# Performance work log

Hardware: AMD Instinct MI355X
Metric: run time of the kernel (lower is better)

## Reference

```python
import jax, jax.numpy as jnp
import numpy as np

D = 1024
H = 16
HD = D // H
B = 4
N = 2048


def setup_inputs() -> dict:
    key = jax.random.key(0)
    ks = jax.random.split(key, 5)
    x = jax.random.normal(ks[0], (B, N, D), dtype=jnp.float32)
    # nn.Linear(D, 3D): weight [3D, D], bias [3D]; y = x @ W.T + b
    w_qkv = jax.random.normal(ks[1], (3 * D, D), dtype=jnp.float32) * (1.0 / np.sqrt(D))
    b_qkv = jax.random.normal(ks[2], (3 * D,), dtype=jnp.float32) * 0.02
    w_out = jax.random.normal(ks[3], (D, D), dtype=jnp.float32) * (1.0 / np.sqrt(D))
    b_out = jax.random.normal(ks[4], (D,), dtype=jnp.float32) * 0.02
    return {"x": x, "w_qkv": w_qkv, "b_qkv": b_qkv, "w_out": w_out, "b_out": b_out}


def reference(x, w_qkv, b_qkv, w_out, b_out):
    Bn, Nn, Dn = x.shape
    scale = HD ** (-0.5)
    qkv = x @ w_qkv.T + b_qkv                      # [B, N, 3D]
    q, k, v = jnp.split(qkv, 3, axis=-1)
    # [B, N, D] -> [B, H, N, HD]
    def heads(t):
        return t.reshape(Bn, Nn, H, HD).transpose(0, 2, 1, 3)
    q, k, v = heads(q), heads(k), heads(v)
    scores = jnp.einsum('bhqd,bhkd->bhqk', q, k) * scale   # [B, H, N, N]
    causal = jnp.tril(jnp.ones((Nn, Nn), dtype=bool))
    scores = jnp.where(causal[None, None], scores, jnp.float32(-jnp.inf))
    alpha = jax.nn.softmax(scores, axis=-1)
    out = jnp.einsum('bhqk,bhkd->bhqd', alpha, v)          # [B, H, N, HD]
    out = out.transpose(0, 2, 1, 3).reshape(Bn, Nn, Dn)
    return out @ w_out.T + b_out
```

## Files before the change

kernel.cpp:

```cpp
#include <hip/hip_runtime.h>
#include <hip/hip_bf16.h>

#define D_MODEL 1024
#define H_HEADS 16
#define HD 64
#define B_BATCH 4
#define N_SEQ 2048
#define BH (B_BATCH*H_HEADS)
#define M_TOT (B_BATCH*N_SEQ)
#define N_QKV (3*D_MODEL)
#define QSCALE 0.18033688011112042f

typedef __bf16 bf16x8 __attribute__((ext_vector_type(8)));
typedef __bf16 bf16x4 __attribute__((ext_vector_type(4)));
typedef float f32x4 __attribute__((ext_vector_type(4)));

#define MFMA16 __builtin_amdgcn_mfma_f32_16x16x32_bf16

__device__ inline ushort cvt_bf16(float f){
  return __builtin_bit_cast(ushort, (__bf16)f);
}

#define GLOAD_LDS16(g, l) __builtin_amdgcn_global_load_lds( \
    (const __attribute__((address_space(1))) void*)(g), \
    (__attribute__((address_space(3))) void*)(l), 16, 0, 0)

__global__ void cvt_f32_bf16_kernel(const float* __restrict__ src, ushort* __restrict__ dst, int n){
  int i = (blockIdx.x*blockDim.x + threadIdx.x)*4;
  int stride = gridDim.x*blockDim.x*4;
  for (; i < n; i += stride){
    float4 f = *reinterpret_cast<const float4*>(src+i);
    ushort4 u;
    u.x=cvt_bf16(f.x); u.y=cvt_bf16(f.y); u.z=cvt_bf16(f.z); u.w=cvt_bf16(f.w);
    *reinterpret_cast<ushort4*>(dst+i) = u;
  }
}

template<int MODE, int MR>
__global__ __launch_bounds__(512,1) void gemm4p(
    const ushort* __restrict__ A, const ushort* __restrict__ Wt,
    const float* __restrict__ bias, void* __restrict__ out,
    int M, int Ncols, int K)
{
  constexpr int BM = MR*32;
  constexpr int BN = 256;
  constexpr int A_SR = BM/2;
  constexpr int A_ISS = BM/128;
  constexpr int VN = 2*A_ISS + 2;
  __shared__ __align__(16) ushort As[2][2][A_SR][64];
  __shared__ __align__(16) ushort Bs[2][2][128][64];
  const int tid = threadIdx.x;
  const int w = tid>>6, lane = tid&63;
  const int wm = w>>2, wn = w&3;
  const int lr = lane&15, lk = lane>>4;

  const int nx = Ncols/BN;
  const int q8 = gridDim.x>>3;
  const int gid = (blockIdx.x&7)*q8 + (blockIdx.x>>3);
  const int bx = gid % nx, by = gid / nx;
  const int row0 = by*BM, col0 = bx*BN;

  const int s_sr8 = lane>>3;
  const int s_cl  = (lane&7) ^ s_sr8;
  const int s_dr  = s_cl>>2;
  const int s_dc  = (s_cl&3)*8;

  auto stageA = [&](int buf, int kt, int ks){
    #pragma unroll
    for (int i=0;i<A_ISS;i++){
      const int sr0 = (w*A_ISS + i)*8;
      GLOAD_LDS16(&A[(size_t)(row0 + 2*(sr0 + s_sr8) + s_dr)*K + kt*64 + ks*32 + s_dc],
                  &As[buf][ks][sr0][0]);
    }
  };
  auto stageB = [&](int buf, int kt, int ks){
    #pragma unroll
    for (int i=0;i<2;i++){
      const int sr0 = (w*2 + i)*8;
      GLOAD_LDS16(&Wt[(size_t)(col0 + 2*(sr0 + s_sr8) + s_dr)*K + kt*64 + ks*32 + s_dc],
                  &Bs[buf][ks][sr0][0]);
    }
  };

  const int rdc = (((lr&1)*4 + lk) ^ ((lr>>1)&7)) * 8;
  f32x4 acc[MR][4] = {};

  const int NT = K/64;
  stageA(0,0,0); stageB(0,0,0); stageA(0,0,1); stageB(0,0,1);
  stageA(1,1,0); stageB(1,1,0); stageA(1,1,1);
  asm volatile("s_waitcnt vmcnt(%0)" :: "i"(VN) : "memory");
  __builtin_amdgcn_s_barrier();

  for (int kt=0; kt<NT; ++kt){
    const int cur = kt&1, nb = cur^1;
    bf16x8 af[MR], bfr[2];

    #pragma unroll
    for (int m=0;m<MR;m++)
      af[m] = *reinterpret_cast<const bf16x8*>(&As[cur][0][wm*(MR*8) + m*8 + (lr>>1)][rdc]);
    bfr[0] = *reinterpret_cast<const bf16x8*>(&Bs[cur][0][wn*32 + 0*8 + (lr>>1)][rdc]);
    bfr[1] = *reinterpret_cast<const bf16x8*>(&Bs[cur][0][wn*32 + 1*8 + (lr>>1)][rdc]);
    if (kt+1 < NT) stageB(nb, kt+1, 1);
    __builtin_amdgcn_s_barrier();
    asm volatile("s_waitcnt lgkmcnt(0)" ::: "memory");
    __builtin_amdgcn_sched_barrier(0);
    __builtin_amdgcn_s_setprio(1);
    #pragma unroll
    for (int m=0;m<MR;m++){
      acc[m][0] = MFMA16(af[m], bfr[0], acc[m][0], 0,0,0);
      acc[m][1] = MFMA16(af[m], bfr[1], acc[m][1], 0,0,0);
    }
    __builtin_amdgcn_s_setprio(0);
    __builtin_amdgcn_s_barrier();

    bfr[0] = *reinterpret_cast<const bf16x8*>(&Bs[cur][0][wn*32 + 2*8 + (lr>>1)][rdc]);
    bfr[1] = *reinterpret_cast<const bf16x8*>(&Bs[cur][0][wn*32 + 3*8 + (lr>>1)][rdc]);
    if (kt+2 < NT) stageA(cur, kt+2, 0);
    __builtin_amdgcn_s_barrier();
    asm volatile("s_waitcnt lgkmcnt(0)" ::: "memory");
    __builtin_amdgcn_sched_barrier(0);
    __builtin_amdgcn_s_setprio(1);
    #pragma unroll
    for (int m=0;m<MR;m++){
      acc[m][2] = MFMA16(af[m], bfr[0], acc[m][2], 0,0,0);
      acc[m][3] = MFMA16(af[m], bfr[1], acc[m][3], 0,0,0);
    }
    __builtin_amdgcn_s_setprio(0);
    __builtin_amdgcn_s_barrier();

    #pragma unroll
    for (int m=0;m<MR;m++)
      af[m] = *reinterpret_cast<const bf16x8*>(&As[cur][1][wm*(MR*8) + m*8 + (lr>>1)][rdc]);
    bfr[0] = *reinterpret_cast<const bf16x8*>(&Bs[cur][1][wn*32 + 0*8 + (lr>>1)][rdc]);
    bfr[1] = *reinterpret_cast<const bf16x8*>(&Bs[cur][1][wn*32 + 1*8 + (lr>>1)][rdc]);
    if (kt+2 < NT) stageB(cur, kt+2, 0);
    __builtin_amdgcn_s_barrier();
    asm volatile("s_waitcnt lgkmcnt(0)" ::: "memory");
    __builtin_amdgcn_sched_barrier(0);
    __builtin_amdgcn_s_setprio(1);
    #pragma unroll
    for (int m=0;m<MR;m++){
      acc[m][0] = MFMA16(af[m], bfr[0], acc[m][0], 0,0,0);
      acc[m][1] = MFMA16(af[m], bfr[1], acc[m][1], 0,0,0);
    }
    __builtin_amdgcn_s_setprio(0);
    __builtin_amdgcn_s_barrier();

    bfr[0] = *reinterpret_cast<const bf16x8*>(&Bs[cur][1][wn*32 + 2*8 + (lr>>1)][rdc]);
    bfr[1] = *reinterpret_cast<const bf16x8*>(&Bs[cur][1][wn*32 + 3*8 + (lr>>1)][rdc]);
    if (kt+2 < NT) stageA(cur, kt+2, 1);
    __builtin_amdgcn_s_barrier();
    asm volatile("s_waitcnt lgkmcnt(0)" ::: "memory");
    __builtin_amdgcn_sched_barrier(0);
    __builtin_amdgcn_s_setprio(1);
    #pragma unroll
    for (int m=0;m<MR;m++){
      acc[m][2] = MFMA16(af[m], bfr[0], acc[m][2], 0,0,0);
      acc[m][3] = MFMA16(af[m], bfr[1], acc[m][3], 0,0,0);
    }
    __builtin_amdgcn_s_setprio(0);
    if (kt < NT-2) asm volatile("s_waitcnt vmcnt(%0)" :: "i"(VN) : "memory");
    else           asm volatile("s_waitcnt vmcnt(0)" ::: "memory");
    __builtin_amdgcn_s_barrier();
  }

  const int ocol_base = col0 + wn*64;
  #pragma unroll
  for (int m=0;m<MR;m++){
    #pragma unroll
    for(int n=0;n<4;n++){
      const int gc = ocol_base + n*16 + lr;
      const float bv = bias[gc];
      const int gr0 = row0 + wm*(MR*16) + m*16 + lk*4;
      float vals[4];
      #pragma unroll
      for (int r=0;r<4;r++) vals[r] = acc[m][n][r] + bv;
      if (MODE==0){
        const int which = gc >> 10;
        const int d = gc & 1023;
        const int h = d >> 6, hd = d & 63;
        const int b = gr0 >> 11, nn0 = gr0 & 2047;
        ushort* o = (ushort*)out;
        if (which==2){
          ushort4 u;
          u.x=cvt_bf16(vals[0]); u.y=cvt_bf16(vals[1]);
          u.z=cvt_bf16(vals[2]); u.w=cvt_bf16(vals[3]);
          *reinterpret_cast<ushort4*>(
            &o[2ull*BH*N_SEQ*HD + ((size_t)(b*H_HEADS+h)*HD + hd)*N_SEQ + nn0]) = u;
        } else {
          const float sc = (which==0) ? QSCALE : 1.0f;
          #pragma unroll
          for (int r=0;r<4;r++)
            o[(size_t)which*((size_t)BH*N_SEQ*HD)
              + ((size_t)(b*H_HEADS+h)*N_SEQ + nn0 + r)*HD + hd] = cvt_bf16(vals[r]*sc);
        }
      } else {
        #pragma unroll
        for (int r=0;r<4;r++)
          ((float*)out)[(size_t)(gr0+r)*Ncols + gc] = vals[r];
      }
    }
  }
}

__global__ __launch_bounds__(256,3) void attn_mfma(
    const ushort* __restrict__ q, const ushort* __restrict__ kg, const ushort* __restrict__ vtg,
    ushort* __restrict__ attn_out)
{
  __shared__ __align__(16) ushort Ks[2][64][64];
  __shared__ __align__(16) ushort Vs[2][64][64];
  __shared__ __align__(16) ushort Ps[4][32][72];
  const int tid=threadIdx.x, w=tid>>6, lane=tid&63;
  const int lr=lane&15, lk=lane>>4;
  const int bid = blockIdx.x;
  const int strip = 15 - (bid>>6);
  const int bh = bid & 63;
  const size_t base=(size_t)bh*N_SEQ*HD;
  const ushort* kb = kg + base;
  const ushort* vb = vtg + base;
  const int b = bh>>4, h = bh&15;

  const int s_roff = lane>>3;
  const int s_g    = (lane&7) ^ s_roff;
  int rd_base[2];
  #pragma unroll
  for (int ks=0;ks<2;ks++)
    rd_base[ks] = lr*64 + (((ks*4+lk) ^ (lr&7))*8);

  const int row0 = strip*128;
  const int wrow = row0 + w*32;
  const int nt = 2*strip + 2;

  bf16x8 qf[2][2];
  #pragma unroll
  for (int qt=0;qt<2;qt++)
    #pragma unroll
    for (int ks=0;ks<2;ks++)
      qf[qt][ks] = *reinterpret_cast<const bf16x8*>(
          &q[base + (size_t)(wrow + qt*16 + lr)*HD + ks*32 + lk*8]);

  f32x4 o_acc[2][4] = {};
  float mrun[2] = {-1e30f,-1e30f}, lrun[2] = {0.f,0.f};

  {
    const int r0k = w*16, rA = r0k + s_roff;
    GLOAD_LDS16(&kb[(size_t)(rA)*HD + s_g*8],       &Ks[0][r0k][0]);
    GLOAD_LDS16(&kb[(size_t)(rA+8)*HD + s_g*8],     &Ks[0][r0k+8][0]);
    GLOAD_LDS16(&vb[(size_t)(rA)*N_SEQ + s_g*8],    &Vs[0][r0k][0]);
    GLOAD_LDS16(&vb[(size_t)(rA+8)*N_SEQ + s_g*8],  &Vs[0][r0k+8][0]);
  }
  int cur = 0;
  for (int t=0;t<nt;t++){
    __syncthreads();
    if (t+1 < nt){
      const int j1 = (t+1)*64;
      const int r0k = w*16, rA = r0k + s_roff;
      GLOAD_LDS16(&kb[(size_t)(j1+rA)*HD + s_g*8],        &Ks[cur^1][r0k][0]);
      GLOAD_LDS16(&kb[(size_t)(j1+rA+8)*HD + s_g*8],      &Ks[cur^1][r0k+8][0]);
      GLOAD_LDS16(&vb[(size_t)(rA)*N_SEQ + j1 + s_g*8],   &Vs[cur^1][r0k][0]);
      GLOAD_LDS16(&vb[(size_t)(rA+8)*N_SEQ + j1 + s_g*8], &Vs[cur^1][r0k+8][0]);
    }
    const int j0 = t*64;
    if (j0 <= wrow + 31){
      const ushort* Kt = &Ks[cur][0][0];
      const ushort* Vt = &Vs[cur][0][0];
      f32x4 sacc[2][4] = {};
      __builtin_amdgcn_s_setprio(1);
      #pragma unroll
      for (int ks=0;ks<2;ks++)
        #pragma unroll
        for (int kt=0;kt<4;kt++){
          bf16x8 kf = *reinterpret_cast<const bf16x8*>(Kt + kt*1024 + rd_base[ks]);
          sacc[0][kt] = MFMA16(kf, qf[0][ks], sacc[0][kt], 0,0,0);
          sacc[1][kt] = MFMA16(kf, qf[1][ks], sacc[1][kt], 0,0,0);
        }
      __builtin_amdgcn_s_setprio(0);

      const bool tailmask = (j0 + 63 > wrow);
      #pragma unroll
      for (int qt=0;qt<2;qt++){
        const int qrow = wrow + qt*16 + lr;
        if (tailmask){
          #pragma unroll
          for (int kt=0;kt<4;kt++)
            #pragma unroll
            for (int r=0;r<4;r++)
              if (j0 + kt*16 + lk*4 + r > qrow) sacc[qt][kt][r] = -1e30f;
        }
        float mx = -1e30f;
        #pragma unroll
        for (int kt=0;kt<4;kt++)
          #pragma unroll
          for (int r=0;r<4;r++) mx = fmaxf(mx, sacc[qt][kt][r]);
        mx = fmaxf(mx, __shfl_xor(mx, 16));
        mx = fmaxf(mx, __shfl_xor(mx, 32));
        float mcur = mrun[qt];
        if (__any(mx - mcur > 8.0f)){
          const float mnew = fmaxf(mcur, mx);
          const float corr = exp2f(mcur - mnew);
          mrun[qt] = mnew; mcur = mnew;
          lrun[qt] *= corr;
          #pragma unroll
          for (int dt=0;dt<4;dt++) o_acc[qt][dt] *= corr;
        }
        float sum = 0.f;
        #pragma unroll
        for (int kt=0;kt<4;kt++){
          float p0 = exp2f(sacc[qt][kt][0]-mcur);
          float p1 = exp2f(sacc[qt][kt][1]-mcur);
          float p2 = exp2f(sacc[qt][kt][2]-mcur);
          float p3 = exp2f(sacc[qt][kt][3]-mcur);
          sum += (p0+p1)+(p2+p3);
          bf16x4 pk;
          pk[0]=(__bf16)p0; pk[1]=(__bf16)p1; pk[2]=(__bf16)p2; pk[3]=(__bf16)p3;
          *reinterpret_cast<bf16x4*>(&Ps[w][qt*16+lr][kt*16+lk*4]) = pk;
        }
        lrun[qt] += sum;
      }

      #pragma unroll
      for (int ks=0;ks<2;ks++){
        bf16x8 pa0 = *reinterpret_cast<const bf16x8*>(&Ps[w][lr][ks*32+lk*8]);
        bf16x8 pa1 = *reinterpret_cast<const bf16x8*>(&Ps[w][16+lr][ks*32+lk*8]);
        __builtin_amdgcn_s_setprio(1);
        #pragma unroll
        for (int dt=0;dt<4;dt++){
          bf16x8 vf = *reinterpret_cast<const bf16x8*>(Vt + dt*1024 + rd_base[ks]);
          o_acc[0][dt] = MFMA16(vf, pa0, o_acc[0][dt], 0,0,0);
          o_acc[1][dt] = MFMA16(vf, pa1, o_acc[1][dt], 0,0,0);
        }
        __builtin_amdgcn_s_setprio(0);
      }
    }
    cur ^= 1;
  }

  #pragma unroll
  for (int qt=0;qt<2;qt++){
    float rl = lrun[qt];
    rl += __shfl_xor(rl, 16);
    rl += __shfl_xor(rl, 32);
    const float rinv = 1.0f / rl;
    const size_t rowb = ((size_t)(b*N_SEQ) + wrow + qt*16 + lr)*D_MODEL + h*HD;
    #pragma unroll
    for (int dt=0;dt<4;dt++){
      bf16x4 u;
      u[0]=(__bf16)(o_acc[qt][dt][0]*rinv);
      u[1]=(__bf16)(o_acc[qt][dt][1]*rinv);
      u[2]=(__bf16)(o_acc[qt][dt][2]*rinv);
      u[3]=(__bf16)(o_acc[qt][dt][3]*rinv);
      *reinterpret_cast<bf16x4*>(&attn_out[rowb + dt*16 + lk*4]) = u;
    }
  }
}

extern "C" void kernel_launch(void* const* d_in, const int* in_sizes, int n_in,
                              void* d_out, int out_size, void* d_ws, size_t ws_size,
                              hipStream_t stream){
  const float* x     = (const float*)d_in[0];
  const float* w_qkv = (const float*)d_in[1];
  const float* b_qkv = (const float*)d_in[2];
  const float* w_out = (const float*)d_in[3];
  const float* b_out = (const float*)d_in[4];

  char* ws = (char*)d_ws;
  size_t off = 0;
  ushort* x_bf    = (ushort*)(ws+off); off += (size_t)M_TOT*D_MODEL*2;
  ushort* wqkv_bf = (ushort*)(ws+off); off += (size_t)N_QKV*D_MODEL*2;
  ushort* wout_bf = (ushort*)(ws+off); off += (size_t)D_MODEL*D_MODEL*2;
  ushort* qkv     = (ushort*)(ws+off); off += 3ull*BH*N_SEQ*HD*2;
  ushort* attn_o  = (ushort*)(ws+off); off += (size_t)M_TOT*D_MODEL*2;

  cvt_f32_bf16_kernel<<<1024, 256, 0, stream>>>(x,     x_bf,    M_TOT*D_MODEL);
  cvt_f32_bf16_kernel<<<512,  256, 0, stream>>>(w_qkv, wqkv_bf, N_QKV*D_MODEL);
  cvt_f32_bf16_kernel<<<256,  256, 0, stream>>>(w_out, wout_bf, D_MODEL*D_MODEL);

  gemm4p<0,8><<<384, 512, 0, stream>>>(x_bf, wqkv_bf, b_qkv, qkv, M_TOT, N_QKV, D_MODEL);

  const ushort* qb  = qkv;
  const ushort* kb  = qkv + (size_t)BH*N_SEQ*HD;
  const ushort* vtb = qkv + 2ull*BH*N_SEQ*HD;
  attn_mfma<<<1024, 256, 0, stream>>>(qb, kb, vtb, attn_o);

  gemm4p<2,4><<<256, 512, 0, stream>>>(attn_o, wout_bf, b_out, (float*)d_out, M_TOT, D_MODEL, D_MODEL);
}
```

Before: 189.0 us.

## Switch GEMMs to 32x32x16 MFMA with a simpler double-buffered pipeline

Rewrites both projection GEMMs to use 32x32x16 bf16 MFMA tiles instead of 16x16x32. Each 32x32 output tile needs fewer LDS fragment loads per unit of compute. The K-loop drops from four barrier-separated quarter phases with two-tile prefetch to a two-buffer scheme that prefetches the next K tile while computing the current one, with a single full vmcnt(0) wait per tile. Launch bounds now request two blocks per CU. The risk is less memory latency hiding from the shallower prefetch depth and higher register pressure from the larger accumulators.

```diff
diff --git a/kernel.cpp b/kernel.cpp
--- a/kernel.cpp
+++ b/kernel.cpp
@@ -14,8 +14,10 @@
 typedef __bf16 bf16x8 __attribute__((ext_vector_type(8)));
 typedef __bf16 bf16x4 __attribute__((ext_vector_type(4)));
 typedef float f32x4 __attribute__((ext_vector_type(4)));
+typedef float f32x16 __attribute__((ext_vector_type(16)));
 
 #define MFMA16 __builtin_amdgcn_mfma_f32_16x16x32_bf16
+#define MFMA32 __builtin_amdgcn_mfma_f32_32x32x16_bf16
 
 __device__ inline ushort cvt_bf16(float f){
   return __builtin_bit_cast(ushort, (__bf16)f);
@@ -36,23 +38,21 @@
   }
 }
 
-template<int MODE, int MR>
-__global__ __launch_bounds__(512,1) void gemm4p(
+template<int MODE, int MRT>
+__global__ __launch_bounds__(512,2) void gemm2p(
     const ushort* __restrict__ A, const ushort* __restrict__ Wt,
     const float* __restrict__ bias, void* __restrict__ out,
     int M, int Ncols, int K)
 {
-  constexpr int BM = MR*32;
+  constexpr int BM = MRT*64;
   constexpr int BN = 256;
   constexpr int A_SR = BM/2;
   constexpr int A_ISS = BM/128;
-  constexpr int VN = 2*A_ISS + 2;
   __shared__ __align__(16) ushort As[2][2][A_SR][64];
   __shared__ __align__(16) ushort Bs[2][2][128][64];
   const int tid = threadIdx.x;
   const int w = tid>>6, lane = tid&63;
   const int wm = w>>2, wn = w&3;
-  const int lr = lane&15, lk = lane>>4;
 
   const int nx = Ncols/BN;
   const int q8 = gridDim.x>>3;
@@ -82,122 +82,131 @@
     }
   };
 
-  const int rdc = (((lr&1)*4 + lk) ^ ((lr>>1)&7)) * 8;
-  f32x4 acc[MR][4] = {};
-
+  const int rsr = (lane&31)>>1;
+  const int swz = rsr & 7;
+  const int pk0 = ((((lane&1)<<2) + 0 + (lane>>5)) ^ swz) * 8;
+  const int pk1 = ((((lane&1)<<2) + 2 + (lane>>5)) ^ swz) * 8;
+
+  f32x16 acc[MRT][2] = {};
   const int NT = K/64;
+
   stageA(0,0,0); stageB(0,0,0); stageA(0,0,1); stageB(0,0,1);
-  stageA(1,1,0); stageB(1,1,0); stageA(1,1,1);
-  asm volatile("s_waitcnt vmcnt(%0)" :: "i"(VN) : "memory");
+  asm volatile("s_waitcnt vmcnt(0)" ::: "memory");
   __builtin_amdgcn_s_barrier();
 
-  for (int kt=0; kt<NT; ++kt){
-    const int cur = kt&1, nb = cur^1;
-    bf16x8 af[MR], bfr[2];
-
-    #pragma unroll
-    for (int m=0;m<MR;m++)
-      af[m] = *reinterpret_cast<const bf16x8*>(&As[cur][0][wm*(MR*8) + m*8 + (lr>>1)][rdc]);
-    bfr[0] = *reinterpret_cast<const bf16x8*>(&Bs[cur][0][wn*32 + 0*8 + (lr>>1)][rdc]);
-    bfr[1] = *reinterpret_cast<const bf16x8*>(&Bs[cur][0][wn*32 + 1*8 + (lr>>1)][rdc]);
-    if (kt+1 < NT) stageB(nb, kt+1, 1);
-    __builtin_amdgcn_s_barrier();
+  auto ktbody = [&](int cur, int kt) __attribute__((always_inline)) {
+    const int nb = cur^1;
+    const ushort* Ab0 = &As[cur][0][0][0];
+    const ushort* Ab1 = &As[cur][1][0][0];
+    const ushort* Bb0 = &Bs[cur][0][0][0];
+    const ushort* Bb1 = &Bs[cur][1][0][0];
+    bf16x8 A0[MRT], A1[MRT], B0[2], B1[2];
+    bf16x8 C0[MRT], C1[MRT], D0[2], D1[2];
+    #pragma unroll
+    for (int mt=0;mt<MRT;mt++){
+      const int ao = (wm*(MRT*16) + mt*16 + rsr)*64;
+      A0[mt] = *reinterpret_cast<const bf16x8*>(Ab0 + ao + pk0);
+      A1[mt] = *reinterpret_cast<const bf16x8*>(Ab0 + ao + pk1);
+    }
+    #pragma unroll
+    for (int nt=0;nt<2;nt++){
+      const int bo = (wn*32 + nt*16 + rsr)*64;
+      B0[nt] = *reinterpret_cast<const bf16x8*>(Bb0 + bo + pk0);
+      B1[nt] = *reinterpret_cast<const bf16x8*>(Bb0 + bo + pk1);
+    }
+    if (kt+1 < NT){ stageA(nb, kt+1, 0); stageB(nb, kt+1, 0); }
+    asm volatile("s_waitcnt lgkmcnt(0)" ::: "memory");
+    __builtin_amdgcn_sched_barrier(0);
+    #pragma unroll
+    for (int mt=0;mt<MRT;mt++){
+      const int ao = (wm*(MRT*16) + mt*16 + rsr)*64;
+      C0[mt] = *reinterpret_cast<const bf16x8*>(Ab1 + ao + pk0);
+      C1[mt] = *reinterpret_cast<const bf16x8*>(Ab1 + ao + pk1);
+    }
+    #pragma unroll
+    for (int nt=0;nt<2;nt++){
+      const int bo = (wn*32 + nt*16 + rsr)*64;
+      D0[nt] = *reinterpret_cast<const bf16x8*>(Bb1 + bo + pk0);
+      D1[nt] = *reinterpret_cast<const bf16x8*>(Bb1 + bo + pk1);
+    }
+    if (kt+1 < NT){ stageA(nb, kt+1, 1); stageB(nb, kt+1, 1); }
+    __builtin_amdgcn_sched_barrier(0);
+    __builtin_amdgcn_s_setprio(1);
+    #pragma unroll
+    for (int mt=0;mt<MRT;mt++){
+      acc[mt][0] = MFMA32(A0[mt], B0[0], acc[mt][0], 0,0,0);
+      acc[mt][1] = MFMA32(A0[mt], B0[1], acc[mt][1], 0,0,0);
+    }
+    #pragma unroll
+    for (int mt=0;mt<MRT;mt++){
+      acc[mt][0] = MFMA32(A1[mt], B1[0], acc[mt][0], 0,0,0);
+      acc[mt][1] = MFMA32(A1[mt], B1[1], acc[mt][1], 0,0,0);
+    }
+    __builtin_amdgcn_s_setprio(0);
     asm volatile("s_waitcnt lgkmcnt(0)" ::: "memory");
     __builtin_amdgcn_sched_barrier(0);
     __builtin_amdgcn_s_setprio(1);
     #pragma unroll
-    for (int m=0;m<MR;m++){
-      acc[m][0] = MFMA16(af[m], bfr[0], acc[m][0], 0,0,0);
-      acc[m][1] = MFMA16(af[m], bfr[1], acc[m][1], 0,0,0);
+    for (int mt=0;mt<MRT;mt++){
+      acc[mt][0] = MFMA32(C0[mt], D0[0], acc[mt][0], 0,0,0);
+      acc[mt][1] = MFMA32(C0[mt], D0[1], acc[mt][1], 0,0,0);
+    }
+    #pragma unroll
+    for (int mt=0;mt<MRT;mt++){
+      acc[mt][0] = MFMA32(C1[mt], D1[0], acc[mt][0], 0,0,0);
+      acc[mt][1] = MFMA32(C1[mt], D1[1], acc[mt][1], 0,0,0);
     }
     __builtin_amdgcn_s_setprio(0);
+    asm volatile("s_waitcnt vmcnt(0)" ::: "memory");
     __builtin_amdgcn_s_barrier();
-
-    bfr[0] = *reinterpret_cast<const bf16x8*>(&Bs[cur][0][wn*32 + 2*8 + (lr>>1)][rdc]);
-    bfr[1] = *reinterpret_cast<const bf16x8*>(&Bs[cur][0][wn*32 + 3*8 + (lr>>1)][rdc]);
-    if (kt+2 < NT) stageA(cur, kt+2, 0);
-    __builtin_amdgcn_s_barrier();
-    asm volatile("s_waitcnt lgkmcnt(0)" ::: "memory");
-    __builtin_amdgcn_sched_barrier(0);
-    __builtin_amdgcn_s_setprio(1);
-    #pragma unroll
-    for (int m=0;m<MR;m++){
-      acc[m][2] = MFMA16(af[m], bfr[0], acc[m][2], 0,0,0);
-      acc[m][3] = MFMA16(af[m], bfr[1], acc[m][3], 0,0,0);
-    }
-    __builtin_amdgcn_s_setprio(0);
-    __builtin_amdgcn_s_barrier();
-
-    #pragma unroll
-    for (int m=0;m<MR;m++)
-      af[m] = *reinterpret_cast<const bf16x8*>(&As[cur][1][wm*(MR*8) + m*8 + (lr>>1)][rdc]);
-    bfr[0] = *reinterpret_cast<const bf16x8*>(&Bs[cur][1][wn*32 + 0*8 + (lr>>1)][rdc]);
-    bfr[1] = *reinterpret_cast<const bf16x8*>(&Bs[cur][1][wn*32 + 1*8 + (lr>>1)][rdc]);
-    if (kt+2 < NT) stageB(cur, kt+2, 0);
-    __builtin_amdgcn_s_barrier();
-    asm volatile("s_waitcnt lgkmcnt(0)" ::: "memory");
-    __builtin_amdgcn_sched_barrier(0);
-    __builtin_amdgcn_s_setprio(1);
-    #pragma unroll
-    for (int m=0;m<MR;m++){
-      acc[m][0] = MFMA16(af[m], bfr[0], acc[m][0], 0,0,0);
-      acc[m][1] = MFMA16(af[m], bfr[1], acc[m][1], 0,0,0);
-    }
-    __builtin_amdgcn_s_setprio(0);
-    __builtin_amdgcn_s_barrier();
-
-    bfr[0] = *reinterpret_cast<const bf16x8*>(&Bs[cur][1][wn*32 + 2*8 + (lr>>1)][rdc]);
-    bfr[1] = *reinterpret_cast<const bf16x8*>(&Bs[cur][1][wn*32 + 3*8 + (lr>>1)][rdc]);
-    if (kt+2 < NT) stageA(cur, kt+2, 1);
-    __builtin_amdgcn_s_barrier();
-    asm volatile("s_waitcnt lgkmcnt(0)" ::: "memory");
-    __builtin_amdgcn_sched_barrier(0);
-    __builtin_amdgcn_s_setprio(1);
-    #pragma unroll
-    for (int m=0;m<MR;m++){
-      acc[m][2] = MFMA16(af[m], bfr[0], acc[m][2], 0,0,0);
-      acc[m][3] = MFMA16(af[m], bfr[1], acc[m][3], 0,0,0);
-    }
-    __builtin_amdgcn_s_setprio(0);
-    if (kt < NT-2) asm volatile("s_waitcnt vmcnt(%0)" :: "i"(VN) : "memory");
-    else           asm volatile("s_waitcnt vmcnt(0)" ::: "memory");
-    __builtin_amdgcn_s_barrier();
-  }
-
-  const int ocol_base = col0 + wn*64;
+  };
+
+  for (int kt=0; kt<NT; kt+=2){
+    ktbody(0, kt);
+    ktbody(1, kt+1);
+  }
+
   #pragma unroll
-  for (int m=0;m<MR;m++){
-    #pragma unroll
-    for(int n=0;n<4;n++){
-      const int gc = ocol_base + n*16 + lr;
+  for (int mt=0;mt<MRT;mt++){
+    #pragma unroll
+    for (int nt=0;nt<2;nt++){
+      const int gc = col0 + wn*64 + nt*32 + (lane&31);
       const float bv = bias[gc];
-      const int gr0 = row0 + wm*(MR*16) + m*16 + lk*4;
-      float vals[4];
-      #pragma unroll
-      for (int r=0;r<4;r++) vals[r] = acc[m][n][r] + bv;
+      const int grB = row0 + wm*(MRT*32) + mt*32 + 4*(lane>>5);
       if (MODE==0){
         const int which = gc >> 10;
         const int d = gc & 1023;
         const int h = d >> 6, hd = d & 63;
-        const int b = gr0 >> 11, nn0 = gr0 & 2047;
         ushort* o = (ushort*)out;
-        if (which==2){
-          ushort4 u;
-          u.x=cvt_bf16(vals[0]); u.y=cvt_bf16(vals[1]);
-          u.z=cvt_bf16(vals[2]); u.w=cvt_bf16(vals[3]);
-          *reinterpret_cast<ushort4*>(
-            &o[2ull*BH*N_SEQ*HD + ((size_t)(b*H_HEADS+h)*HD + hd)*N_SEQ + nn0]) = u;
-        } else {
-          const float sc = (which==0) ? QSCALE : 1.0f;
+        #pragma unroll
+        for (int rg=0;rg<4;rg++){
+          const int gr0 = grB + rg*8;
+          const int b = gr0 >> 11, nn0 = gr0 & 2047;
+          if (which==2){
+            ushort4 u;
+            u.x=cvt_bf16(acc[mt][nt][rg*4+0] + bv);
+            u.y=cvt_bf16(acc[mt][nt][rg*4+1] + bv);
+            u.z=cvt_bf16(acc[mt][nt][rg*4+2] + bv);
+            u.w=cvt_bf16(acc[mt][nt][rg*4+3] + bv);
+            *reinterpret_cast<ushort4*>(
+              &o[2ull*BH*N_SEQ*HD + ((size_t)(b*H_HEADS+h)*HD + hd)*N_SEQ + nn0]) = u;
+          } else {
+            const float sc = (which==0) ? QSCALE : 1.0f;
+            #pragma unroll
+            for (int r=0;r<4;r++)
+              o[(size_t)which*((size_t)BH*N_SEQ*HD)
+                + ((size_t)(b*H_HEADS+h)*N_SEQ + nn0 + r)*HD + hd]
+                  = cvt_bf16((acc[mt][nt][rg*4+r] + bv)*sc);
+          }
+        }
+      } else {
+        #pragma unroll
+        for (int rg=0;rg<4;rg++){
+          const int gr0 = grB + rg*8;
           #pragma unroll
           for (int r=0;r<4;r++)
-            o[(size_t)which*((size_t)BH*N_SEQ*HD)
-              + ((size_t)(b*H_HEADS+h)*N_SEQ + nn0 + r)*HD + hd] = cvt_bf16(vals[r]*sc);
-        }
-      } else {
-        #pragma unroll
-        for (int r=0;r<4;r++)
-          ((float*)out)[(size_t)(gr0+r)*Ncols + gc] = vals[r];
+            ((float*)out)[(size_t)(gr0+r)*Ncols + gc] = acc[mt][nt][rg*4+r] + bv;
+        }
       }
     }
   }
@@ -375,12 +384,12 @@
   cvt_f32_bf16_kernel<<<512,  256, 0, stream>>>(w_qkv, wqkv_bf, N_QKV*D_MODEL);
   cvt_f32_bf16_kernel<<<256,  256, 0, stream>>>(w_out, wout_bf, D_MODEL*D_MODEL);
 
-  gemm4p<0,8><<<384, 512, 0, stream>>>(x_bf, wqkv_bf, b_qkv, qkv, M_TOT, N_QKV, D_MODEL);
+  gemm2p<0,4><<<384, 512, 0, stream>>>(x_bf, wqkv_bf, b_qkv, qkv, M_TOT, N_QKV, D_MODEL);
 
   const ushort* qb  = qkv;
   const ushort* kb  = qkv + (size_t)BH*N_SEQ*HD;
   const ushort* vtb = qkv + 2ull*BH*N_SEQ*HD;
   attn_mfma<<<1024, 256, 0, stream>>>(qb, kb, vtb, attn_o);
 
-  gemm4p<2,4><<<256, 512, 0, stream>>>(attn_o, wout_bf, b_out, (float*)d_out, M_TOT, D_MODEL, D_MODEL);
-}
+  gemm2p<2,2><<<256, 512, 0, stream>>>(attn_o, wout_bf, b_out, (float*)d_out, M_TOT, D_MODEL, D_MODEL);
+}
```

New measurement: 194.4 us. 1.03x slower.

## Use dedicated 256x384-tile QKV GEMM so grid matches one wave of CUs

Applied to the files above, without the earlier changes.

Replaces the templated QKV projection GEMM (256x256 tiles, 384 blocks) with a dedicated kernel using 256x384 tiles and 256 blocks, with each wave computing an 8x6 MFMA accumulator block. K-staging of A and B is interleaved with four MFMA phases per K tile. The aim is to raise arithmetic intensity per LDS load and avoid a partial second wave of blocks on 256 CUs. The trade-off is many more accumulator registers and more LDS per block, which could cause spills or lower latency hiding. The output GEMM is split into its own non-templated kernel with unchanged behaviour.

```diff
diff --git a/kernel.cpp b/kernel.cpp
--- a/kernel.cpp
+++ b/kernel.cpp
@@ -36,12 +36,167 @@
   }
 }
 
-template<int MODE, int MR>
-__global__ __launch_bounds__(512,1) void gemm4p(
+__global__ __launch_bounds__(512,1) void gemm_qkv(
     const ushort* __restrict__ A, const ushort* __restrict__ Wt,
-    const float* __restrict__ bias, void* __restrict__ out,
+    const float* __restrict__ bias, ushort* __restrict__ out, int K)
+{
+  __shared__ __align__(16) ushort As[2][2][128][64];
+  __shared__ __align__(16) ushort Bs[2][2][192][64];
+  const int tid = threadIdx.x;
+  const int w = tid>>6, lane = tid&63;
+  const int wm = w>>2, wn = w&3;
+  const int lr = lane&15, lk = lane>>4;
+
+  const int gid = ((int)blockIdx.x&7)*32 + ((int)blockIdx.x>>3);
+  const int bx = gid & 7, by = gid >> 3;
+  const int row0 = by*256, col0 = bx*384;
+
+  const int s_sr8 = lane>>3;
+  const int s_cl  = (lane&7) ^ s_sr8;
+  const int s_dr  = s_cl>>2;
+  const int s_dc  = (s_cl&3)*8;
+
+  auto stageA = [&](int buf, int kt, int ks){
+    #pragma unroll
+    for (int i=0;i<2;i++){
+      const int sr0 = (w*2 + i)*8;
+      GLOAD_LDS16(&A[(size_t)(row0 + 2*(sr0 + s_sr8) + s_dr)*K + kt*64 + ks*32 + s_dc],
+                  &As[buf][ks][sr0][0]);
+    }
+  };
+  auto stageB = [&](int buf, int kt, int ks){
+    #pragma unroll
+    for (int i=0;i<3;i++){
+      const int sr0 = (w*3 + i)*8;
+      GLOAD_LDS16(&Wt[(size_t)(col0 + 2*(sr0 + s_sr8) + s_dr)*K + kt*64 + ks*32 + s_dc],
+                  &Bs[buf][ks][sr0][0]);
+    }
+  };
+
+  const int rdc = (((lr&1)*4 + lk) ^ ((lr>>1)&7)) * 8;
+  f32x4 acc[8][6] = {};
+  const int NT = K/64;
+
+  stageA(0,0,0); stageB(0,0,0); stageA(0,0,1); stageB(0,0,1);
+  asm volatile("s_waitcnt vmcnt(5)" ::: "memory");
+  __builtin_amdgcn_s_barrier();
+
+  for (int kt=0; kt<NT; ++kt){
+    const int cur = kt&1, nb = cur^1;
+    const bool last = (kt == NT-1);
+    bf16x8 bfr[6], af[4];
+
+    #pragma unroll
+    for (int nt=0;nt<6;nt++)
+      bfr[nt] = *reinterpret_cast<const bf16x8*>(&Bs[cur][0][wn*48 + nt*8 + (lr>>1)][rdc]);
+    #pragma unroll
+    for (int m=0;m<4;m++)
+      af[m] = *reinterpret_cast<const bf16x8*>(&As[cur][0][wm*64 + m*8 + (lr>>1)][rdc]);
+    if (!last) stageA(nb, kt+1, 0);
+    __builtin_amdgcn_s_barrier();
+    asm volatile("s_waitcnt lgkmcnt(0)" ::: "memory");
+    __builtin_amdgcn_sched_barrier(0);
+    __builtin_amdgcn_s_setprio(1);
+    #pragma unroll
+    for (int m=0;m<4;m++)
+      #pragma unroll
+      for (int nt=0;nt<6;nt++)
+        acc[m][nt] = MFMA16(af[m], bfr[nt], acc[m][nt], 0,0,0);
+    __builtin_amdgcn_s_setprio(0);
+    __builtin_amdgcn_s_barrier();
+
+    #pragma unroll
+    for (int m=0;m<4;m++)
+      af[m] = *reinterpret_cast<const bf16x8*>(&As[cur][0][wm*64 + (m+4)*8 + (lr>>1)][rdc]);
+    if (!last) stageB(nb, kt+1, 0);
+    __builtin_amdgcn_s_barrier();
+    asm volatile("s_waitcnt lgkmcnt(0)" ::: "memory");
+    __builtin_amdgcn_sched_barrier(0);
+    __builtin_amdgcn_s_setprio(1);
+    #pragma unroll
+    for (int m=0;m<4;m++)
+      #pragma unroll
+      for (int nt=0;nt<6;nt++)
+        acc[m+4][nt] = MFMA16(af[m], bfr[nt], acc[m+4][nt], 0,0,0);
+    __builtin_amdgcn_s_setprio(0);
+    if (last) asm volatile("s_waitcnt vmcnt(0)" ::: "memory");
+    else      asm volatile("s_waitcnt vmcnt(5)" ::: "memory");
+    __builtin_amdgcn_s_barrier();
+
+    #pragma unroll
+    for (int nt=0;nt<6;nt++)
+      bfr[nt] = *reinterpret_cast<const bf16x8*>(&Bs[cur][1][wn*48 + nt*8 + (lr>>1)][rdc]);
+    #pragma unroll
+    for (int m=0;m<4;m++)
+      af[m] = *reinterpret_cast<const bf16x8*>(&As[cur][1][wm*64 + m*8 + (lr>>1)][rdc]);
+    if (!last) stageA(nb, kt+1, 1);
+    __builtin_amdgcn_s_barrier();
+    asm volatile("s_waitcnt lgkmcnt(0)" ::: "memory");
+    __builtin_amdgcn_sched_barrier(0);
+    __builtin_amdgcn_s_setprio(1);
+    #pragma unroll
+    for (int m=0;m<4;m++)
+      #pragma unroll
+      for (int nt=0;nt<6;nt++)
+        acc[m][nt] = MFMA16(af[m], bfr[nt], acc[m][nt], 0,0,0);
+    __builtin_amdgcn_s_setprio(0);
+    __builtin_amdgcn_s_barrier();
+
+    #pragma unroll
+    for (int m=0;m<4;m++)
+      af[m] = *reinterpret_cast<const bf16x8*>(&As[cur][1][wm*64 + (m+4)*8 + (lr>>1)][rdc]);
+    if (!last) stageB(nb, kt+1, 1);
+    __builtin_amdgcn_s_barrier();
+    asm volatile("s_waitcnt lgkmcnt(0)" ::: "memory");
+    __builtin_amdgcn_sched_barrier(0);
+    __builtin_amdgcn_s_setprio(1);
+    #pragma unroll
+    for (int m=0;m<4;m++)
+      #pragma unroll
+      for (int nt=0;nt<6;nt++)
+        acc[m+4][nt] = MFMA16(af[m], bfr[nt], acc[m+4][nt], 0,0,0);
+    __builtin_amdgcn_s_setprio(0);
+    if (!last) asm volatile("s_waitcnt vmcnt(5)" ::: "memory");
+    __builtin_amdgcn_s_barrier();
+  }
+
+  #pragma unroll
+  for (int m=0;m<8;m++){
+    #pragma unroll
+    for (int nt=0;nt<6;nt++){
+      const int gc = col0 + wn*96 + nt*16 + lr;
+      const float bv = bias[gc];
+      const int gr0 = row0 + wm*128 + m*16 + lk*4;
+      const int which = gc >> 10;
+      const int d = gc & 1023;
+      const int h = d >> 6, hd = d & 63;
+      const int b = gr0 >> 11, nn0 = gr0 & 2047;
+      float vals[4];
+      #pragma unroll
+      for (int r=0;r<4;r++) vals[r] = acc[m][nt][r] + bv;
+      if (which==2){
+        ushort4 u;
+        u.x=cvt_bf16(vals[0]); u.y=cvt_bf16(vals[1]);
+        u.z=cvt_bf16(vals[2]); u.w=cvt_bf16(vals[3]);
+        *reinterpret_cast<ushort4*>(
+          &out[2ull*BH*N_SEQ*HD + ((size_t)(b*H_HEADS+h)*HD + hd)*N_SEQ + nn0]) = u;
+      } else {
+        const float sc = (which==0) ? QSCALE : 1.0f;
+        #pragma unroll
+        for (int r=0;r<4;r++)
+          out[(size_t)which*((size_t)BH*N_SEQ*HD)
+            + ((size_t)(b*H_HEADS+h)*N_SEQ + nn0 + r)*HD + hd] = cvt_bf16(vals[r]*sc);
+      }
+    }
+  }
+}
+
+__global__ __launch_bounds__(512,1) void gemm_out(
+    const ushort* __restrict__ A, const ushort* __restrict__ Wt,
+    const float* __restrict__ bias, float* __restrict__ out,
     int M, int Ncols, int K)
 {
+  constexpr int MR = 4;
   constexpr int BM = MR*32;
   constexpr int BN = 256;
   constexpr int A_SR = BM/2;
@@ -172,33 +327,9 @@
       const int gc = ocol_base + n*16 + lr;
       const float bv = bias[gc];
       const int gr0 = row0 + wm*(MR*16) + m*16 + lk*4;
-      float vals[4];
-      #pragma unroll
-      for (int r=0;r<4;r++) vals[r] = acc[m][n][r] + bv;
-      if (MODE==0){
-        const int which = gc >> 10;
-        const int d = gc & 1023;
-        const int h = d >> 6, hd = d & 63;
-        const int b = gr0 >> 11, nn0 = gr0 & 2047;
-        ushort* o = (ushort*)out;
-        if (which==2){
-          ushort4 u;
-          u.x=cvt_bf16(vals[0]); u.y=cvt_bf16(vals[1]);
-          u.z=cvt_bf16(vals[2]); u.w=cvt_bf16(vals[3]);
-          *reinterpret_cast<ushort4*>(
-            &o[2ull*BH*N_SEQ*HD + ((size_t)(b*H_HEADS+h)*HD + hd)*N_SEQ + nn0]) = u;
-        } else {
-          const float sc = (which==0) ? QSCALE : 1.0f;
-          #pragma unroll
-          for (int r=0;r<4;r++)
-            o[(size_t)which*((size_t)BH*N_SEQ*HD)
-              + ((size_t)(b*H_HEADS+h)*N_SEQ + nn0 + r)*HD + hd] = cvt_bf16(vals[r]*sc);
-        }
-      } else {
-        #pragma unroll
-        for (int r=0;r<4;r++)
-          ((float*)out)[(size_t)(gr0+r)*Ncols + gc] = vals[r];
-      }
+      #pragma unroll
+      for (int r=0;r<4;r++)
+        out[(size_t)(gr0+r)*Ncols + gc] = acc[m][n][r] + bv;
     }
   }
 }
@@ -375,12 +506,12 @@
   cvt_f32_bf16_kernel<<<512,  256, 0, stream>>>(w_qkv, wqkv_bf, N_QKV*D_MODEL);
   cvt_f32_bf16_kernel<<<256,  256, 0, stream>>>(w_out, wout_bf, D_MODEL*D_MODEL);
 
-  gemm4p<0,8><<<384, 512, 0, stream>>>(x_bf, wqkv_bf, b_qkv, qkv, M_TOT, N_QKV, D_MODEL);
+  gemm_qkv<<<256, 512, 0, stream>>>(x_bf, wqkv_bf, b_qkv, qkv, D_MODEL);
 
   const ushort* qb  = qkv;
   const ushort* kb  = qkv + (size_t)BH*N_SEQ*HD;
   const ushort* vtb = qkv + 2ull*BH*N_SEQ*HD;
   attn_mfma<<<1024, 256, 0, stream>>>(qb, kb, vtb, attn_o);
 
-  gemm4p<2,4><<<256, 512, 0, stream>>>(attn_o, wout_bf, b_out, (float*)d_out, M_TOT, D_MODEL, D_MODEL);
+  gemm_out<<<256, 512, 0, stream>>>(attn_o, wout_bf, b_out, (float*)d_out, M_TOT, D_MODEL, D_MODEL);
 }
```

Result: faster. 182.5 us (-3.4%).
